# Optimization experiments

Hardware: AMD Instinct MI355X
Metric: run time of the kernel (lower is better)

The kernel has to match this reference:

```python
import jax, jax.numpy as jnp
import numpy as np

N, M, D_IN, D_OUT = 8192, 8192, 512, 512


def setup_inputs() -> dict:
    key = jax.random.key(0)
    k1, k2, k3, k4 = jax.random.split(key, 4)
    return {
        "x": jax.random.normal(k1, (N, D_OUT), dtype=jnp.float32),
        "mu": jax.random.normal(k2, (M, D_IN), dtype=jnp.float32),
        "W": jax.random.normal(k3, (D_OUT, D_IN), dtype=jnp.float32),
        "b": jax.random.normal(k4, (D_OUT,), dtype=jnp.float32),
    }


def reference(x, mu, W, b):
    # f_mu: (M, D_out) -- projection + nonlinearity (func = tanh)
    f_mu = jnp.tanh(mu @ W.T + b)
    # measure m[n, m] = -0.5 * ||x_n - f_mu_m||^2, via the matmul expansion
    # (avoids the (N, M, D) diff tensor; same math as sum of squared diffs)
    x_sq = jnp.sum(x * x, axis=-1)            # (N,)
    f_sq = jnp.sum(f_mu * f_mu, axis=-1)      # (M,)
    cross = x @ f_mu.T                        # (N, M)
    m = -0.5 * (x_sq[:, None] - 2.0 * cross + f_sq[None, :])
    # energy: -sum over rows of logsumexp over axis 1
    return -jnp.sum(jax.nn.logsumexp(m, axis=1))
```

## Files before the change

### kernel.cpp

```cpp
#include <hip/hip_runtime.h>

#define D 512
#define NROWS 8192
#define MROWS 8192
#define NCHUNK 8
#define CHUNK_COLS (MROWS / NCHUNK)
#define SWEEPS (CHUNK_COLS / 256)
#define NRB (NROWS / 128)
#define LOG2E 1.4426950408889634f
#define LN2 0.6931471805599453f

typedef float floatx4 __attribute__((ext_vector_type(4)));
typedef __bf16 bf16x8 __attribute__((ext_vector_type(8)));
typedef unsigned uintx4 __attribute__((ext_vector_type(4)));

typedef __attribute__((address_space(1))) void* as1_void_p;
typedef __attribute__((address_space(3))) void* as3_void_p;

__device__ __forceinline__ void async_cp16(const void* g, void* l) {
    __builtin_amdgcn_global_load_lds((as1_void_p)(void*)g, (as3_void_p)l, 16, 0, 0);
}

__device__ __forceinline__ unsigned short f2bf(float f) {
    unsigned u = __float_as_uint(f);
    u += 0x7fffu + ((u >> 16) & 1u);
    return (unsigned short)(u >> 16);
}
__device__ __forceinline__ float bf2f(unsigned short h) {
    return __uint_as_float(((unsigned)h) << 16);
}

__device__ __forceinline__ float fast_tanh(float x) {
    const float xc = fminf(fmaxf(x, -15.0f), 15.0f);
    const float e = __builtin_exp2f(xc * (2.0f * LOG2E));
    return (e - 1.0f) * __builtin_amdgcn_rcpf(e + 1.0f);
}

__device__ __forceinline__ unsigned pack2(float a, float b) {
    return (unsigned)f2bf(a) | ((unsigned)f2bf(b) << 16);
}

#define XBLK (NROWS / 4)
#define MUBLK (MROWS * D / 2048)
#define WBLK (D * D / 2048)
__global__ void k_prep(const float* __restrict__ x,
                       const float* __restrict__ mu,
                       const float* __restrict__ W,
                       unsigned short* __restrict__ xb,
                       unsigned short* __restrict__ mub,
                       unsigned short* __restrict__ Wb,
                       float* __restrict__ xsq,
                       float* __restrict__ fsq,
                       float* __restrict__ out) {
    const int bid = blockIdx.x;
    const int t = threadIdx.x;
    if (bid < XBLK) {
        if (bid == 0 && t == 0) out[0] = 0.f;
        const int row = bid * 4 + (t >> 6);
        const int lane = t & 63;
        const float4 v0 = ((const float4*)(x + (size_t)row * D))[lane * 2];
        const float4 v1 = ((const float4*)(x + (size_t)row * D))[lane * 2 + 1];
        uintx4 o;
        o.x = pack2(v0.x * LOG2E, v0.y * LOG2E);
        o.y = pack2(v0.z * LOG2E, v0.w * LOG2E);
        o.z = pack2(v1.x * LOG2E, v1.y * LOG2E);
        o.w = pack2(v1.z * LOG2E, v1.w * LOG2E);
        ((uintx4*)(xb + (size_t)row * D))[lane] = o;
        float s = v0.x * v0.x + v0.y * v0.y + v0.z * v0.z + v0.w * v0.w
                + v1.x * v1.x + v1.y * v1.y + v1.z * v1.z + v1.w * v1.w;
        #pragma unroll
        for (int m = 1; m < 64; m <<= 1) s += __shfl_xor(s, m);
        if (lane == 0) xsq[row] = s;
    } else if (bid < XBLK + MUBLK) {
        const size_t i = ((size_t)(bid - XBLK) * 256 + t) * 2;
        const float4 v0 = ((const float4*)mu)[i];
        const float4 v1 = ((const float4*)mu)[i + 1];
        uintx4 o;
        o.x = pack2(v0.x, v0.y); o.y = pack2(v0.z, v0.w);
        o.z = pack2(v1.x, v1.y); o.w = pack2(v1.z, v1.w);
        ((uintx4*)mub)[i / 2] = o;
    } else {
        const int wb = bid - XBLK - MUBLK;
        const size_t i = ((size_t)wb * 256 + t) * 2;
        const float4 v0 = ((const float4*)W)[i];
        const float4 v1 = ((const float4*)W)[i + 1];
        uintx4 o;
        o.x = pack2(v0.x, v0.y); o.y = pack2(v0.z, v0.w);
        o.z = pack2(v1.x, v1.y); o.w = pack2(v1.z, v1.w);
        ((uintx4*)Wb)[i / 2] = o;
        if (t < 64) fsq[wb * 64 + t] = 0.f;
    }
}

__global__ __launch_bounds__(256, 2)
void k_fgemm(const unsigned short* __restrict__ mub,
             const unsigned short* __restrict__ Wb,
             const float* __restrict__ bias,
             unsigned short* __restrict__ fb,
             float* __restrict__ fsq) {
    __shared__ unsigned short Ab[128 * 32];
    __shared__ unsigned short Bb[128 * 32];

    const int tid = threadIdx.x;
    const int wave = tid >> 6;
    const int lane = tid & 63;
    const int wr = wave >> 1, wc = wave & 1;
    const int g = lane >> 4;
    const int lm = lane & 15;

    const int row0 = blockIdx.x * 128;
    const int col0 = blockIdx.y * 128;

    const int srow = tid >> 2;
    const int gsrc = (tid & 3) ^ ((srow >> 1) & 3);
    const unsigned short* gA = mub + (size_t)(row0 + srow) * D + gsrc * 8;
    const unsigned short* gB = Wb  + (size_t)(col0 + srow) * D + gsrc * 8;
    char* lA = ((char*)Ab) + wave * 1024;
    char* lB = ((char*)Bb) + wave * 1024;

    const int xsel = (lm >> 1) & 3;
    const unsigned short* fragA = Ab + (64 * wr + lm) * 32 + (g ^ xsel) * 8;
    const unsigned short* fragB = Bb + (64 * wc + lm) * 32 + (g ^ xsel) * 8;

    floatx4 acc[4][4];
    const floatx4 zz = {0.f, 0.f, 0.f, 0.f};
    #pragma unroll
    for (int i = 0; i < 4; ++i)
        #pragma unroll
        for (int j = 0; j < 4; ++j) acc[i][j] = zz;

    for (int kt = 0; kt < 16; ++kt) {
        const int k0 = kt * 32;
        async_cp16(gA + k0, lA);
        async_cp16(gA + 64 * D + k0, lA + 4096);
        async_cp16(gB + k0, lB);
        async_cp16(gB + 64 * D + k0, lB + 4096);
        __syncthreads();
        bf16x8 af[4], bfr[4];
        #pragma unroll
        for (int i = 0; i < 4; ++i) af[i] = *(const bf16x8*)(fragA + i * 512);
        #pragma unroll
        for (int j = 0; j < 4; ++j) bfr[j] = *(const bf16x8*)(fragB + j * 512);
        #pragma unroll
        for (int i = 0; i < 4; ++i)
            #pragma unroll
            for (int j = 0; j < 4; ++j)
                acc[i][j] = __builtin_amdgcn_mfma_f32_16x16x32_bf16(af[i], bfr[j], acc[i][j], 0, 0, 0);
        __syncthreads();
    }

    float bcol[4];
    #pragma unroll
    for (int j = 0; j < 4; ++j) bcol[j] = bias[col0 + 64 * wc + 16 * j + lm];
    #pragma unroll
    for (int i = 0; i < 4; ++i) {
        #pragma unroll
        for (int r = 0; r < 4; ++r) {
            const int row = row0 + 64 * wr + 16 * i + 4 * g + r;
            float sq = 0.f;
            #pragma unroll
            for (int j = 0; j < 4; ++j) {
                const int col = col0 + 64 * wc + 16 * j + lm;
                const unsigned short h = f2bf(fast_tanh(acc[i][j][r] + bcol[j]));
                fb[(size_t)row * D + col] = h;
                const float fr = bf2f(h);
                sq += fr * fr;
            }
            #pragma unroll
            for (int d = 1; d < 16; d <<= 1) sq += __shfl_xor(sq, d);
            if (lm == 0) atomicAdd(fsq + row, sq);
        }
    }
}

__global__ __launch_bounds__(256, 2)
void k_cross(const unsigned short* __restrict__ xb,
             const unsigned short* __restrict__ fb,
             const float* __restrict__ fsq,
             float* __restrict__ pmax,
             float* __restrict__ psum) {
    __shared__ unsigned short Ab[128 * 32];
    __shared__ unsigned short Bb[256 * 32];
    __shared__ float mbuf[128], sbuf[128];

    const int tid = threadIdx.x;
    const int wave = tid >> 6;
    const int lane = tid & 63;
    const int wr = wave >> 1, wc = wave & 1;
    const int g = lane >> 4;
    const int lm = lane & 15;

    const int row0 = blockIdx.x * 128;
    const int chunk = blockIdx.y;

    const int srow = tid >> 2;
    const int gsrc = (tid & 3) ^ ((srow >> 1) & 3);
    const unsigned short* gA = xb + (size_t)(row0 + srow) * D + gsrc * 8;
    char* lA = ((char*)Ab) + wave * 1024;
    char* lB = ((char*)Bb) + wave * 1024;

    const int xsel = (lm >> 1) & 3;
    const unsigned short* fragA = Ab + (64 * wr + lm) * 32 + (g ^ xsel) * 8;
    const unsigned short* fragB = Bb + (128 * wc + lm) * 32 + (g ^ xsel) * 8;

    float m_loc[4][4], s_loc[4][4];
    #pragma unroll
    for (int i = 0; i < 4; ++i)
        #pragma unroll
        for (int r = 0; r < 4; ++r) { m_loc[i][r] = -__builtin_inff(); s_loc[i][r] = 0.f; }

    for (int st = 0; st < SWEEPS; ++st) {
        const int col0 = chunk * CHUNK_COLS + st * 256;
        const unsigned short* gB = fb + (size_t)(col0 + srow) * D + gsrc * 8;

        floatx4 acc[4][8];
        const floatx4 zz = {0.f, 0.f, 0.f, 0.f};
        #pragma unroll
        for (int i = 0; i < 4; ++i)
            #pragma unroll
            for (int j = 0; j < 8; ++j) acc[i][j] = zz;

        for (int kt = 0; kt < 16; ++kt) {
            const int k0 = kt * 32;
            async_cp16(gA + k0, lA);
            async_cp16(gA + 64 * D + k0, lA + 4096);
            #pragma unroll
            for (int h = 0; h < 4; ++h)
                async_cp16(gB + (size_t)(64 * h) * D + k0, lB + 4096 * h);
            __syncthreads();
            bf16x8 af[4];
            #pragma unroll
            for (int i = 0; i < 4; ++i) af[i] = *(const bf16x8*)(fragA + i * 512);
            #pragma unroll
            for (int j = 0; j < 8; ++j) {
                const bf16x8 bj = *(const bf16x8*)(fragB + j * 512);
                acc[0][j] = __builtin_amdgcn_mfma_f32_16x16x32_bf16(af[0], bj, acc[0][j], 0, 0, 0);
                acc[1][j] = __builtin_amdgcn_mfma_f32_16x16x32_bf16(af[1], bj, acc[1][j], 0, 0, 0);
                acc[2][j] = __builtin_amdgcn_mfma_f32_16x16x32_bf16(af[2], bj, acc[2][j], 0, 0, 0);
                acc[3][j] = __builtin_amdgcn_mfma_f32_16x16x32_bf16(af[3], bj, acc[3][j], 0, 0, 0);
            }
            __syncthreads();
        }

        float hf[8];
        #pragma unroll
        for (int j = 0; j < 8; ++j)
            hf[j] = 0.5f * LOG2E * fsq[col0 + 128 * wc + 16 * j + lm];
        #pragma unroll
        for (int i = 0; i < 4; ++i) {
            #pragma unroll
            for (int r = 0; r < 4; ++r) {
                float v[8];
                float mm = -__builtin_inff();
                #pragma unroll
                for (int j = 0; j < 8; ++j) {
                    v[j] = acc[i][j][r] - hf[j];
                    mm = fmaxf(mm, v[j]);
                }
                const float nm = fmaxf(m_loc[i][r], mm);
                float s = s_loc[i][r] * __builtin_exp2f(m_loc[i][r] - nm);
                #pragma unroll
                for (int j = 0; j < 8; ++j) s += __builtin_exp2f(v[j] - nm);
                s_loc[i][r] = s;
                m_loc[i][r] = nm;
            }
        }
    }

    #pragma unroll
    for (int i = 0; i < 4; ++i) {
        #pragma unroll
        for (int r = 0; r < 4; ++r) {
            float m = m_loc[i][r], s = s_loc[i][r];
            #pragma unroll
            for (int d = 1; d < 16; d <<= 1) {
                const float om = __shfl_xor(m, d);
                const float os = __shfl_xor(s, d);
                const float nm = fmaxf(m, om);
                s = s * __builtin_exp2f(m - nm) + os * __builtin_exp2f(om - nm);
                m = nm;
            }
            m_loc[i][r] = m; s_loc[i][r] = s;
        }
    }
    if (wc == 0 && lm == 0) {
        #pragma unroll
        for (int i = 0; i < 4; ++i)
            #pragma unroll
            for (int r = 0; r < 4; ++r) {
                const int rl = 64 * wr + 16 * i + 4 * g + r;
                mbuf[rl] = m_loc[i][r]; sbuf[rl] = s_loc[i][r];
            }
    }
    __syncthreads();
    if (wc == 1 && lm == 0) {
        #pragma unroll
        for (int i = 0; i < 4; ++i)
            #pragma unroll
            for (int r = 0; r < 4; ++r) {
                const int rl = 64 * wr + 16 * i + 4 * g + r;
                const float om = mbuf[rl], os = sbuf[rl];
                float m = m_loc[i][r], s = s_loc[i][r];
                const float nm = fmaxf(m, om);
                s = s * __builtin_exp2f(m - nm) + os * __builtin_exp2f(om - nm);
                pmax[(size_t)(row0 + rl) * NCHUNK + chunk] = nm;
                psum[(size_t)(row0 + rl) * NCHUNK + chunk] = s;
            }
    }
}

__global__ void k_finish(const float* __restrict__ pmax,
                         const float* __restrict__ psum,
                         const float* __restrict__ xsq,
                         float* __restrict__ out) {
    const int row = blockIdx.x * 256 + threadIdx.x;
    const float4* pm4 = (const float4*)(pmax + (size_t)row * NCHUNK);
    const float4* ps4 = (const float4*)(psum + (size_t)row * NCHUNK);
    float pm[NCHUNK], ps[NCHUNK];
    #pragma unroll
    for (int c = 0; c < NCHUNK / 4; ++c) {
        const float4 a = pm4[c], b = ps4[c];
        pm[4*c] = a.x; pm[4*c+1] = a.y; pm[4*c+2] = a.z; pm[4*c+3] = a.w;
        ps[4*c] = b.x; ps[4*c+1] = b.y; ps[4*c+2] = b.z; ps[4*c+3] = b.w;
    }
    float gm = -__builtin_inff();
    #pragma unroll
    for (int c = 0; c < NCHUNK; ++c) gm = fmaxf(gm, pm[c]);
    float s = 0.f;
    #pragma unroll
    for (int c = 0; c < NCHUNK; ++c) s += ps[c] * __builtin_exp2f(pm[c] - gm);
    float lse = LN2 * (gm + __builtin_log2f(s)) - 0.5f * xsq[row];
    #pragma unroll
    for (int m = 1; m < 64; m <<= 1) lse += __shfl_xor(lse, m);
    __shared__ float ws4[4];
    if ((threadIdx.x & 63) == 0) ws4[threadIdx.x >> 6] = lse;
    __syncthreads();
    if (threadIdx.x == 0) atomicAdd(out, -(ws4[0] + ws4[1] + ws4[2] + ws4[3]));
}

extern "C" void kernel_launch(void* const* d_in, const int* in_sizes, int n_in,
                              void* d_out, int out_size, void* d_ws, size_t ws_size,
                              hipStream_t stream) {
    const float* x  = (const float*)d_in[0];
    const float* mu = (const float*)d_in[1];
    const float* W  = (const float*)d_in[2];
    const float* b  = (const float*)d_in[3];

    char* ws = (char*)d_ws;
    unsigned short* xb  = (unsigned short*)(ws);
    unsigned short* fb  = (unsigned short*)(ws + (8u << 20));
    unsigned short* mub = (unsigned short*)(ws + (16u << 20));
    unsigned short* Wb  = (unsigned short*)(ws + (24u << 20));
    float* xsq  = (float*)(ws + (25u << 20));
    float* fsq  = xsq + NROWS;
    float* pmax = fsq + MROWS;
    float* psum = pmax + (size_t)NROWS * NCHUNK;

    float* out = (float*)d_out;

    hipLaunchKernelGGL(k_prep, dim3(XBLK + MUBLK + WBLK), dim3(256), 0, stream,
                       x, mu, W, xb, mub, Wb, xsq, fsq, out);
    hipLaunchKernelGGL(k_fgemm, dim3(MROWS / 128, D / 128), dim3(256), 0, stream,
                       mub, Wb, b, fb, fsq);
    hipLaunchKernelGGL(k_cross, dim3(NRB, NCHUNK), dim3(256), 0, stream,
                       xb, fb, fsq, pmax, psum);
    hipLaunchKernelGGL(k_finish, dim3(NROWS / 256), dim3(256), 0, stream,
                       pmax, psum, xsq, out);
}
```

Baseline: 182.6 us.

## Halve fgemm column tile and double k-step per barrier in cross GEMM

The f_mu GEMM now uses 128x64 tiles instead of 128x128, doubling its grid to 512 blocks so more CUs have work. In the cross GEMM, each barrier pair now covers a K-step of 64 instead of 32, staged through two LDS buffers, which halves the number of __syncthreads per sweep. The cost is double the LDS use in k_cross (about 49KB), which may reduce occupancy, plus lower data reuse per block in fgemm.

```diff
diff --git a/kernel.cpp b/kernel.cpp
--- a/kernel.cpp
+++ b/kernel.cpp
@@ -99,7 +99,7 @@
              unsigned short* __restrict__ fb,
              float* __restrict__ fsq) {
     __shared__ unsigned short Ab[128 * 32];
-    __shared__ unsigned short Bb[128 * 32];
+    __shared__ unsigned short Bb[64 * 32];
 
     const int tid = threadIdx.x;
     const int wave = tid >> 6;
@@ -109,7 +109,7 @@
     const int lm = lane & 15;
 
     const int row0 = blockIdx.x * 128;
-    const int col0 = blockIdx.y * 128;
+    const int col0 = blockIdx.y * 64;
 
     const int srow = tid >> 2;
     const int gsrc = (tid & 3) ^ ((srow >> 1) & 3);
@@ -120,38 +120,37 @@
 
     const int xsel = (lm >> 1) & 3;
     const unsigned short* fragA = Ab + (64 * wr + lm) * 32 + (g ^ xsel) * 8;
-    const unsigned short* fragB = Bb + (64 * wc + lm) * 32 + (g ^ xsel) * 8;
-
-    floatx4 acc[4][4];
+    const unsigned short* fragB = Bb + (32 * wc + lm) * 32 + (g ^ xsel) * 8;
+
+    floatx4 acc[4][2];
     const floatx4 zz = {0.f, 0.f, 0.f, 0.f};
     #pragma unroll
     for (int i = 0; i < 4; ++i)
         #pragma unroll
-        for (int j = 0; j < 4; ++j) acc[i][j] = zz;
+        for (int j = 0; j < 2; ++j) acc[i][j] = zz;
 
     for (int kt = 0; kt < 16; ++kt) {
         const int k0 = kt * 32;
         async_cp16(gA + k0, lA);
         async_cp16(gA + 64 * D + k0, lA + 4096);
         async_cp16(gB + k0, lB);
-        async_cp16(gB + 64 * D + k0, lB + 4096);
         __syncthreads();
-        bf16x8 af[4], bfr[4];
+        bf16x8 af[4], bfr[2];
         #pragma unroll
         for (int i = 0; i < 4; ++i) af[i] = *(const bf16x8*)(fragA + i * 512);
         #pragma unroll
-        for (int j = 0; j < 4; ++j) bfr[j] = *(const bf16x8*)(fragB + j * 512);
+        for (int j = 0; j < 2; ++j) bfr[j] = *(const bf16x8*)(fragB + j * 512);
         #pragma unroll
         for (int i = 0; i < 4; ++i)
             #pragma unroll
-            for (int j = 0; j < 4; ++j)
+            for (int j = 0; j < 2; ++j)
                 acc[i][j] = __builtin_amdgcn_mfma_f32_16x16x32_bf16(af[i], bfr[j], acc[i][j], 0, 0, 0);
         __syncthreads();
     }
 
-    float bcol[4];
-    #pragma unroll
-    for (int j = 0; j < 4; ++j) bcol[j] = bias[col0 + 64 * wc + 16 * j + lm];
+    float bcol[2];
+    #pragma unroll
+    for (int j = 0; j < 2; ++j) bcol[j] = bias[col0 + 32 * wc + 16 * j + lm];
     #pragma unroll
     for (int i = 0; i < 4; ++i) {
         #pragma unroll
@@ -159,8 +158,8 @@
             const int row = row0 + 64 * wr + 16 * i + 4 * g + r;
             float sq = 0.f;
             #pragma unroll
-            for (int j = 0; j < 4; ++j) {
-                const int col = col0 + 64 * wc + 16 * j + lm;
+            for (int j = 0; j < 2; ++j) {
+                const int col = col0 + 32 * wc + 16 * j + lm;
                 const unsigned short h = f2bf(fast_tanh(acc[i][j][r] + bcol[j]));
                 fb[(size_t)row * D + col] = h;
                 const float fr = bf2f(h);
@@ -179,8 +178,8 @@
              const float* __restrict__ fsq,
              float* __restrict__ pmax,
              float* __restrict__ psum) {
-    __shared__ unsigned short Ab[128 * 32];
-    __shared__ unsigned short Bb[256 * 32];
+    __shared__ unsigned short Ab[2][128 * 32];
+    __shared__ unsigned short Bb[2][256 * 32];
     __shared__ float mbuf[128], sbuf[128];
 
     const int tid = threadIdx.x;
@@ -196,12 +195,14 @@
     const int srow = tid >> 2;
     const int gsrc = (tid & 3) ^ ((srow >> 1) & 3);
     const unsigned short* gA = xb + (size_t)(row0 + srow) * D + gsrc * 8;
-    char* lA = ((char*)Ab) + wave * 1024;
-    char* lB = ((char*)Bb) + wave * 1024;
+    char* lA0 = ((char*)Ab[0]) + wave * 1024;
+    char* lA1 = ((char*)Ab[1]) + wave * 1024;
+    char* lB0 = ((char*)Bb[0]) + wave * 1024;
+    char* lB1 = ((char*)Bb[1]) + wave * 1024;
 
     const int xsel = (lm >> 1) & 3;
-    const unsigned short* fragA = Ab + (64 * wr + lm) * 32 + (g ^ xsel) * 8;
-    const unsigned short* fragB = Bb + (128 * wc + lm) * 32 + (g ^ xsel) * 8;
+    const unsigned short* fragA0 = Ab[0] + (64 * wr + lm) * 32 + (g ^ xsel) * 8;
+    const unsigned short* fragB0 = Bb[0] + (128 * wc + lm) * 32 + (g ^ xsel) * 8;
 
     float m_loc[4][4], s_loc[4][4];
     #pragma unroll
@@ -220,24 +221,33 @@
             #pragma unroll
             for (int j = 0; j < 8; ++j) acc[i][j] = zz;
 
-        for (int kt = 0; kt < 16; ++kt) {
-            const int k0 = kt * 32;
-            async_cp16(gA + k0, lA);
-            async_cp16(gA + 64 * D + k0, lA + 4096);
-            #pragma unroll
-            for (int h = 0; h < 4; ++h)
-                async_cp16(gB + (size_t)(64 * h) * D + k0, lB + 4096 * h);
+        for (int kt = 0; kt < 8; ++kt) {
+            const int k0 = kt * 64;
+            async_cp16(gA + k0, lA0);
+            async_cp16(gA + 64 * D + k0, lA0 + 4096);
+            async_cp16(gA + k0 + 32, lA1);
+            async_cp16(gA + 64 * D + k0 + 32, lA1 + 4096);
+            #pragma unroll
+            for (int h = 0; h < 4; ++h) {
+                async_cp16(gB + (size_t)(64 * h) * D + k0, lB0 + 4096 * h);
+                async_cp16(gB + (size_t)(64 * h) * D + k0 + 32, lB1 + 4096 * h);
+            }
             __syncthreads();
-            bf16x8 af[4];
-            #pragma unroll
-            for (int i = 0; i < 4; ++i) af[i] = *(const bf16x8*)(fragA + i * 512);
-            #pragma unroll
-            for (int j = 0; j < 8; ++j) {
-                const bf16x8 bj = *(const bf16x8*)(fragB + j * 512);
-                acc[0][j] = __builtin_amdgcn_mfma_f32_16x16x32_bf16(af[0], bj, acc[0][j], 0, 0, 0);
-                acc[1][j] = __builtin_amdgcn_mfma_f32_16x16x32_bf16(af[1], bj, acc[1][j], 0, 0, 0);
-                acc[2][j] = __builtin_amdgcn_mfma_f32_16x16x32_bf16(af[2], bj, acc[2][j], 0, 0, 0);
-                acc[3][j] = __builtin_amdgcn_mfma_f32_16x16x32_bf16(af[3], bj, acc[3][j], 0, 0, 0);
+            #pragma unroll
+            for (int h = 0; h < 2; ++h) {
+                const unsigned short* fA = fragA0 + h * 4096;
+                const unsigned short* fB = fragB0 + h * 8192;
+                bf16x8 af[4];
+                #pragma unroll
+                for (int i = 0; i < 4; ++i) af[i] = *(const bf16x8*)(fA + i * 512);
+                #pragma unroll
+                for (int j = 0; j < 8; ++j) {
+                    const bf16x8 bj = *(const bf16x8*)(fB + j * 512);
+                    acc[0][j] = __builtin_amdgcn_mfma_f32_16x16x32_bf16(af[0], bj, acc[0][j], 0, 0, 0);
+                    acc[1][j] = __builtin_amdgcn_mfma_f32_16x16x32_bf16(af[1], bj, acc[1][j], 0, 0, 0);
+                    acc[2][j] = __builtin_amdgcn_mfma_f32_16x16x32_bf16(af[2], bj, acc[2][j], 0, 0, 0);
+                    acc[3][j] = __builtin_amdgcn_mfma_f32_16x16x32_bf16(af[3], bj, acc[3][j], 0, 0, 0);
+                }
             }
             __syncthreads();
         }
@@ -360,7 +370,7 @@
 
     hipLaunchKernelGGL(k_prep, dim3(XBLK + MUBLK + WBLK), dim3(256), 0, stream,
                        x, mu, W, xb, mub, Wb, xsq, fsq, out);
-    hipLaunchKernelGGL(k_fgemm, dim3(MROWS / 128, D / 128), dim3(256), 0, stream,
+    hipLaunchKernelGGL(k_fgemm, dim3(MROWS / 128, D / 64), dim3(256), 0, stream,
                        mub, Wb, b, fb, fsq);
     hipLaunchKernelGGL(k_cross, dim3(NRB, NCHUNK), dim3(256), 0, stream,
                        xb, fb, fsq, pmax, psum);
```

Measured after the change: 172.4 us. -5.5%, faster.
